# Kernel tuning notes

Hardware: AMD Instinct MI355X
Metric: run time of the kernel (lower is better)

## Reference

```python
import jax, jax.numpy as jnp
import numpy as np

H, D, G, P = 8, 64, 64, 3
ROPE_BASE = 10000.0

def _gelu(x):
    return jax.nn.gelu(x, approximate=False)  # torch nn.GELU default (erf)

def setup_inputs() -> dict:
    key = jax.random.key(0)
    ks = jax.random.split(key, 20)
    B, N, C = 2, 32768, 256
    inner = H * D
    s = 0.02
    inp = {
        'x': jax.random.normal(ks[0], (B, N, C), jnp.float32),
        'pos': jax.random.uniform(ks[1], (B, N, P), jnp.float32),
        'gumbel_u': jax.random.uniform(ks[2], (B, H, N, G), jnp.float32),
        'Wx': jax.random.normal(ks[3], (C, inner), jnp.float32) * s,
        'bx': jnp.zeros((inner,), jnp.float32),
        'W1': jax.random.normal(ks[4], (D, G), jnp.float32) * s,   # proj_temperature[0]
        'b1': jnp.zeros((G,), jnp.float32),
        'W2': jax.random.normal(ks[5], (G, 1), jnp.float32) * s,   # proj_temperature[2]
        'b2': jnp.zeros((1,), jnp.float32),
        'bias': jnp.full((1, H, 1, 1), 0.5, jnp.float32),
        'Wr': jax.random.normal(ks[6], (2 * P, D), jnp.float32) * s,  # rope_projection
        'br': jnp.zeros((D,), jnp.float32),
        'Ws': jax.random.normal(ks[7], (D, G), jnp.float32) * s,   # in_project_slice
        'bs': jnp.zeros((G,), jnp.float32),
        'Wq': jax.random.normal(ks[8], (D, D), jnp.float32) * s,
        'Wk': jax.random.normal(ks[9], (D, D), jnp.float32) * s,
        'Wv': jax.random.normal(ks[10], (D, D), jnp.float32) * s,
        'Wg1': jax.random.normal(ks[11], (2 * D, D), jnp.float32) * s,  # attn_gate[0]
        'bg1': jnp.zeros((D,), jnp.float32),
        'Wg2': jax.random.normal(ks[12], (D, D), jnp.float32) * s,      # attn_gate[2]
        'bg2': jnp.zeros((D,), jnp.float32),
        'Wo': jax.random.normal(ks[13], (inner, C), jnp.float32) * s,   # to_out
        'bo': jnp.zeros((C,), jnp.float32),
    }
    return inp

def reference(x, pos, gumbel_u, Wx, bx, W1, b1, W2, b2, bias, Wr, br, Ws, bs,
              Wq, Wk, Wv, Wg1, bg1, Wg2, bg2, Wo, bo):
    B, N, C = x.shape
    dt = x.dtype
    # project and split heads: [B,H,N,D]
    x_mid = (x @ Wx + bx).reshape(B, N, H, D).transpose(0, 2, 1, 3)
    # RoPE features: sin/cos of pos * inv_freq, projected to dim_head
    inv_freq = jnp.exp(-jnp.arange(P, dtype=dt) * jnp.log(jnp.asarray(ROPE_BASE, dt)) / P)
    ang = pos[..., :P] * inv_freq                                  # [B,N,P]
    rope_feat = jnp.concatenate([jnp.sin(ang), jnp.cos(ang)], -1)  # [B,N,2P]
    x_mid = x_mid + (rope_feat @ Wr + br)[:, None]                 # broadcast over heads
    # per-token temperature, clamped
    temp = _gelu(_gelu(x_mid @ W1 + b1) @ W2 + b2) + bias          # [B,H,N,1]
    temp = jnp.maximum(temp, 0.01)
    # gumbel-softmax slice weights (soft, hard=False)
    logits = x_mid @ Ws + bs                                       # [B,H,N,G]
    gnoise = -jnp.log(-jnp.log(gumbel_u + 1e-8) + 1e-8)
    sw = jax.nn.softmax((logits + gnoise) / temp, axis=-1)
    # pool N tokens into G slice tokens
    snorm = sw.sum(axis=2)                                         # [B,H,G]
    st = jnp.einsum('bhnc,bhng->bhgc', x_mid, sw) / (snorm + 1e-5)[..., None]
    # tiny SDPA over G learned tokens
    q, k, v = st @ Wq, st @ Wk, st @ Wv
    attn = jax.nn.softmax(jnp.einsum('bhgc,bhkc->bhgk', q, k) / jnp.sqrt(jnp.asarray(D, dt)), axis=-1)
    out_st = jnp.einsum('bhgk,bhkc->bhgc', attn, v)
    # sigmoid gate
    gate_in = jnp.concatenate([st, out_st], axis=-1)               # [B,H,G,2D]
    gate = jax.nn.sigmoid(jax.nn.silu(gate_in @ Wg1 + bg1) @ Wg2 + bg2)
    out_st = gate * out_st
    # broadcast slice tokens back to N tokens
    out_x = jnp.einsum('bhgc,bhng->bhnc', out_st, sw)
    out_x = out_x.transpose(0, 2, 1, 3).reshape(B, N, H * D)
    return out_x @ Wo + bo
```

## Files before the change

kernel.cpp:

```cpp
#include <hip/hip_runtime.h>
#include <math.h>

#define NSEQ 32768

using short8v = __attribute__((ext_vector_type(8))) short;
using f32x4   = __attribute__((ext_vector_type(4))) float;
#define MFMA16 __builtin_amdgcn_mfma_f32_16x16x32_bf16

__device__ __forceinline__ unsigned short f2bf(float f){
  union{float f; unsigned u;} v; v.f = f;
  return (unsigned short)((v.u + 0x7FFFu + ((v.u>>16)&1u))>>16);
}
__device__ __forceinline__ float bf2f(unsigned short h){
  union{unsigned u; float f;} v; v.u = ((unsigned)h)<<16; return v.f;
}
__device__ __forceinline__ void split2(float f, unsigned short* h, unsigned short* l){
  unsigned short hh = f2bf(f);
  *h = hh; *l = f2bf(f - bf2f(hh));
}
__device__ __forceinline__ float gelu_f(float x){
  return 0.5f*x*(1.f + erff(x*0.70710678118654752f));
}

__global__ __launch_bounds__(256) void k0_prep(const float* __restrict__ Wx,
    unsigned short* __restrict__ WxTH, unsigned short* __restrict__ WxTL)
{
  const int n = blockIdx.x;
  const int k = threadIdx.x;
  float v = Wx[(size_t)k*512 + n];
  unsigned short hh, ll; split2(v,&hh,&ll);
  WxTH[n*256+k]=hh; WxTL[n*256+k]=ll;
}

__global__ __launch_bounds__(256) void k0b_prep(
  const float* __restrict__ Wq, const float* __restrict__ Wk, const float* __restrict__ Wv,
  const float* __restrict__ Wg1, const float* __restrict__ Wg2, const float* __restrict__ Wo,
  const float* __restrict__ W1, const float* __restrict__ Ws,
  unsigned short* __restrict__ WqTH, unsigned short* __restrict__ WqTL,
  unsigned short* __restrict__ WkTH, unsigned short* __restrict__ WkTL,
  unsigned short* __restrict__ WvTH, unsigned short* __restrict__ WvTL,
  unsigned short* __restrict__ Wg1TH, unsigned short* __restrict__ Wg1TL,
  unsigned short* __restrict__ Wg2TH, unsigned short* __restrict__ Wg2TL,
  unsigned short* __restrict__ WoTH, unsigned short* __restrict__ WoTL,
  unsigned short* __restrict__ W1TH, unsigned short* __restrict__ W1TL,
  unsigned short* __restrict__ WsTH, unsigned short* __restrict__ WsTL)
{
  const int bx = blockIdx.x, t = threadIdx.x;
  unsigned short hh, ll;
  if (bx == 0){
    for (int i=0;i<16;i++){ int idx=i*256+t; int r=idx>>6, c=idx&63;
      split2(Wq[r*64+c],&hh,&ll); WqTH[c*64+r]=hh; WqTL[c*64+r]=ll;
      split2(Wk[r*64+c],&hh,&ll); WkTH[c*64+r]=hh; WkTL[c*64+r]=ll;
      split2(Wv[r*64+c],&hh,&ll); WvTH[c*64+r]=hh; WvTL[c*64+r]=ll;
    }
  } else if (bx == 1){
    for (int i=0;i<32;i++){ int idx=i*256+t; int r=idx>>6, c=idx&63;
      split2(Wg1[r*64+c],&hh,&ll); Wg1TH[c*128+r]=hh; Wg1TL[c*128+r]=ll;
    }
  } else if (bx == 2){
    for (int i=0;i<16;i++){ int idx=i*256+t; int r=idx>>6, c=idx&63;
      split2(Wg2[r*64+c],&hh,&ll); Wg2TH[c*64+r]=hh; Wg2TL[c*64+r]=ll;
      split2(W1[r*64+c],&hh,&ll);  W1TH[c*64+r]=hh;  W1TL[c*64+r]=ll;
      split2(Ws[r*64+c],&hh,&ll);  WsTH[c*64+r]=hh;  WsTL[c*64+r]=ll;
    }
  } else {
    int kb = (bx-3)*64;
    for (int i=0;i<64;i++){ int k = kb+i;
      split2(Wo[(size_t)k*256 + t],&hh,&ll);
      WoTH[(size_t)t*512 + k]=hh; WoTL[(size_t)t*512 + k]=ll;
    }
  }
}

__global__ __launch_bounds__(512,1) void k1_gemm_rope(
    const float* __restrict__ x, const float* __restrict__ pos,
    const unsigned short* __restrict__ WxTH, const unsigned short* __restrict__ WxTL,
    const float* __restrict__ bx,
    const float* __restrict__ Wr, const float* __restrict__ br,
    float* __restrict__ xmid)
{
  __shared__ unsigned short SA[2*128*128];
  __shared__ unsigned short SB[2*64*128];
  __shared__ float trig[128][8];
  const int tid = threadIdx.x;
  const int wave = tid>>6, lane = tid&63, l15 = lane&15, lq = lane>>4;
  const int m0 = blockIdx.x*128;

  if (tid < 128){
    int m = m0 + tid;
    float a0 = pos[m*3+0];
    float a1 = pos[m*3+1] * 0.046415888336127774f;
    float a2 = pos[m*3+2] * 0.002154434690031884f;
    trig[tid][0]=sinf(a0); trig[tid][1]=sinf(a1); trig[tid][2]=sinf(a2);
    trig[tid][3]=cosf(a0); trig[tid][4]=cosf(a1); trig[tid][5]=cosf(a2);
  }

  short8v aHr[8], aLr[8];
  {
    const int lm = tid>>2, lkq = (tid&3)*32;
    #pragma unroll
    for (int kh=0; kh<2; kh++){
      __syncthreads();
      const float* src = x + (size_t)(m0+lm)*256 + kh*128 + lkq;
      #pragma unroll
      for (int i=0;i<8;i++){
        float4 v = *(const float4*)(src + i*4);
        ushort4 hh, ll;
        split2(v.x,&hh.x,&ll.x); split2(v.y,&hh.y,&ll.y);
        split2(v.z,&hh.z,&ll.z); split2(v.w,&hh.w,&ll.w);
        int G = (lkq>>3) + (i>>1);
        int idx = lm*128 + (((G ^ (lm&15)))<<3) + ((i&1)<<2);
        *(ushort4*)&SA[idx] = hh;
        *(ushort4*)&SA[128*128 + idx] = ll;
      }
      __syncthreads();
      const int row = wave*16 + l15;
      #pragma unroll
      for (int ks=0; ks<4; ks++){
        int idx = row*128 + ((((ks<<2)+lq) ^ l15)<<3);
        aHr[kh*4+ks] = *(const short8v*)&SA[idx];
        aLr[kh*4+ks] = *(const short8v*)&SA[128*128 + idx];
      }
    }
  }

  float ropev[4][4];
  #pragma unroll
  for (int r=0;r<4;r++){
    int tk = wave*16 + lq*4 + r;
    float t0=trig[tk][0],t1=trig[tk][1],t2=trig[tk][2];
    float t3=trig[tk][3],t4=trig[tk][4],t5=trig[tk][5];
    #pragma unroll
    for (int j=0;j<4;j++){
      int d = j*16 + l15;
      float v = br[d];
      v = fmaf(t0, Wr[0*64+d], v);
      v = fmaf(t1, Wr[1*64+d], v);
      v = fmaf(t2, Wr[2*64+d], v);
      v = fmaf(t3, Wr[3*64+d], v);
      v = fmaf(t4, Wr[4*64+d], v);
      v = fmaf(t5, Wr[5*64+d], v);
      ropev[r][j] = v;
    }
  }

  const int bidx = m0 >> 15;
  const int nbase = (m0 & 32767) + wave*16 + lq*4;
  const int ln = tid>>3, lnkq = (tid&7)*16;

  for (int h=0; h<8; h++){
    f32x4 acc[4] = {};
    #pragma unroll
    for (int kh=0; kh<2; kh++){
      __syncthreads();
      {
        const unsigned short* sH = WxTH + (size_t)(h*64+ln)*256 + kh*128 + lnkq;
        const unsigned short* sL = WxTL + (size_t)(h*64+ln)*256 + kh*128 + lnkq;
        int g0 = lnkq>>3;
        int i0 = ln*128 + ((g0     ^ (ln&15))<<3);
        int i1 = ln*128 + (((g0+1) ^ (ln&15))<<3);
        *(uint4*)&SB[i0] = *(const uint4*)sH;
        *(uint4*)&SB[i1] = *(const uint4*)(sH+8);
        *(uint4*)&SB[64*128 + i0] = *(const uint4*)sL;
        *(uint4*)&SB[64*128 + i1] = *(const uint4*)(sL+8);
      }
      __syncthreads();
      #pragma unroll
      for (int ks=0; ks<4; ks++){
        short8v a_h = aHr[kh*4+ks], a_l = aLr[kh*4+ks];
        #pragma unroll
        for (int j=0;j<4;j++){
          int idx = (j*16+l15)*128 + ((((ks<<2)+lq) ^ l15)<<3);
          short8v b_h = *(const short8v*)&SB[idx];
          short8v b_l = *(const short8v*)&SB[64*128 + idx];
          acc[j] = MFMA16(a_h,b_h,acc[j],0,0,0);
          acc[j] = MFMA16(a_h,b_l,acc[j],0,0,0);
          acc[j] = MFMA16(a_l,b_h,acc[j],0,0,0);
        }
      }
    }
    #pragma unroll
    for (int j=0;j<4;j++){
      int col = j*16 + l15;
      float bxv = bx[h*64+col];
      #pragma unroll
      for (int r=0;r<4;r++){
        xmid[(((size_t)(bidx*8+h))*NSEQ + nbase + r)*64 + col] =
          acc[j][r] + bxv + ropev[r][j];
      }
    }
  }
}

__global__ __launch_bounds__(512,1) void k2_tile(
  const float* __restrict__ xmid, const float* __restrict__ gum,
  const unsigned short* __restrict__ W1TH, const unsigned short* __restrict__ W1TL,
  const float* __restrict__ b1,
  const float* __restrict__ W2, const float* __restrict__ b2,
  const float* __restrict__ biasp,
  const unsigned short* __restrict__ WsTH, const unsigned short* __restrict__ WsTL,
  const float* __restrict__ bs,
  unsigned* __restrict__ swT, float* __restrict__ part)
{
  __shared__ unsigned short XAh[128*72], XAl[128*72];
  __shared__ unsigned short XBh[64*136], XBl[64*136];
  __shared__ unsigned short swh[64*136], swl[64*136];
  __shared__ float snred[8*64];
  __shared__ float prm[200];

  const int tid = threadIdx.x;
  const int wave = tid>>6, lane = tid&63, l15 = lane&15, lq = lane>>4;
  const int bh = blockIdx.y, chunk = blockIdx.x, h = bh&7;
  const size_t rowbase = (size_t)bh*NSEQ;

  if (tid<64){ prm[tid]=b1[tid]; prm[64+tid]=bs[tid]; prm[128+tid]=W2[tid]; }
  if (tid==64){ prm[192]=b2[0]; prm[193]=biasp[h]; }

  f32x4 acc2[2] = {};
  float snacc[4][4] = {};
  const int gt2 = wave>>1, dbase = (wave&1)*2;

  for (int sub=0; sub<4; ++sub){
    const int n0 = chunk*512 + sub*128;
    __syncthreads();
    {
      const int lm = tid>>2, ldq = (tid&3)*16;
      const float* src = xmid + (rowbase + n0 + lm)*64 + ldq;
      #pragma unroll
      for (int i=0;i<4;i++){
        float4 v = *(const float4*)(src + i*4);
        float vv[4]={v.x,v.y,v.z,v.w};
        ushort4 hh, ll;
        unsigned short* hp=(unsigned short*)&hh; unsigned short* lp=(unsigned short*)&ll;
        #pragma unroll
        for (int j=0;j<4;j++) split2(vv[j], &hp[j], &lp[j]);
        *(ushort4*)&XAh[lm*72 + ldq + i*4] = hh;
        *(ushort4*)&XAl[lm*72 + ldq + i*4] = ll;
        #pragma unroll
        for (int j=0;j<4;j++){
          XBh[(ldq+i*4+j)*136 + lm] = hp[j];
          XBl[(ldq+i*4+j)*136 + lm] = lp[j];
        }
      }
    }
    __syncthreads();

    const int mloc = wave*16 + l15;
    const float* grow = gum + (rowbase + n0 + mloc)*64;
    float4 gu[4];
    #pragma unroll
    for (int gt=0; gt<4; gt++) gu[gt] = *(const float4*)(grow + gt*16 + lq*4);

    f32x4 t1a[4] = {}, lga[4] = {};
    #pragma unroll
    for (int ks=0; ks<2; ks++){
      const int koff = ks*32 + lq*8;
      short8v xH = *(const short8v*)&XAh[(wave*16+l15)*72 + koff];
      short8v xL = *(const short8v*)&XAl[(wave*16+l15)*72 + koff];
      #pragma unroll
      for (int gt=0; gt<4; gt++){
        const int woff = (gt*16+l15)*64 + koff;
        short8v wH = *(const short8v*)(W1TH + woff);
        short8v wL = *(const short8v*)(W1TL + woff);
        t1a[gt] = MFMA16(wH,xH,t1a[gt],0,0,0);
        t1a[gt] = MFMA16(wH,xL,t1a[gt],0,0,0);
        t1a[gt] = MFMA16(wL,xH,t1a[gt],0,0,0);
        short8v sH = *(const short8v*)(WsTH + woff);
        short8v sL = *(const short8v*)(WsTL + woff);
        lga[gt] = MFMA16(sH,xH,lga[gt],0,0,0);
        lga[gt] = MFMA16(sH,xL,lga[gt],0,0,0);
        lga[gt] = MFMA16(sL,xH,lga[gt],0,0,0);
      }
    }

    float p = 0.f;
    #pragma unroll
    for (int gt=0; gt<4; gt++)
      #pragma unroll
      for (int r=0;r<4;r++){
        int g = gt*16 + lq*4 + r;
        p += gelu_f(t1a[gt][r] + prm[g]) * prm[128+g];
      }
    p += __shfl_xor(p,16); p += __shfl_xor(p,32);
    float t2 = gelu_f(p + prm[192]);
    float rtemp = 1.f / fmaxf(t2 + prm[193], 0.01f);

    float z[4][4]; float mx = -1e30f;
    #pragma unroll
    for (int gt=0; gt<4; gt++){
      float guv[4] = {gu[gt].x, gu[gt].y, gu[gt].z, gu[gt].w};
      #pragma unroll
      for (int r=0;r<4;r++){
        int g = gt*16 + lq*4 + r;
        float gn = -__logf(-__logf(guv[r]+1e-8f)+1e-8f);
        float zz = (lga[gt][r] + prm[64+g] + gn)*rtemp;
        z[gt][r]=zz; mx = fmaxf(mx, zz);
      }
    }
    mx = fmaxf(mx, __shfl_xor(mx,16)); mx = fmaxf(mx, __shfl_xor(mx,32));
    float se = 0.f;
    #pragma unroll
    for (int gt=0; gt<4; gt++)
      #pragma unroll
      for (int r=0;r<4;r++){ float e = __expf(z[gt][r]-mx); z[gt][r]=e; se += e; }
    se += __shfl_xor(se,16); se += __shfl_xor(se,32);
    float inv = 1.f/se;
    #pragma unroll
    for (int gt=0; gt<4; gt++)
      #pragma unroll
      for (int r=0;r<4;r++){
        float swv = z[gt][r]*inv;
        snacc[gt][r] += swv;
        int g = gt*16 + lq*4 + r;
        unsigned short hh,ll; split2(swv,&hh,&ll);
        swh[g*136 + mloc] = hh; swl[g*136 + mloc] = ll;
      }
    __syncthreads();

    {
      const int g = tid>>3, mq = (tid&7)*16;
      #pragma unroll
      for (int i=0;i<4;i++){
        ushort4 hh = *(const ushort4*)&swh[g*136 + mq + i*4];
        ushort4 ll = *(const ushort4*)&swl[g*136 + mq + i*4];
        uint4 pk;
        pk.x = (unsigned)hh.x | ((unsigned)ll.x<<16);
        pk.y = (unsigned)hh.y | ((unsigned)ll.y<<16);
        pk.z = (unsigned)hh.z | ((unsigned)ll.z<<16);
        pk.w = (unsigned)hh.w | ((unsigned)ll.w<<16);
        *(uint4*)(swT + ((size_t)bh*64 + g)*NSEQ + n0 + mq + i*4) = pk;
      }
    }

    #pragma unroll
    for (int ks=0; ks<4; ks++){
      const int koff = ks*32 + lq*8;
      short8v aH = *(const short8v*)&swh[(gt2*16+l15)*136 + koff];
      short8v aL = *(const short8v*)&swl[(gt2*16+l15)*136 + koff];
      #pragma unroll
      for (int dt=0; dt<2; dt++){
        const int boff = ((dbase+dt)*16+l15)*136 + koff;
        short8v bH = *(const short8v*)&XBh[boff];
        short8v bL = *(const short8v*)&XBl[boff];
        acc2[dt] = MFMA16(aH,bH,acc2[dt],0,0,0);
        acc2[dt] = MFMA16(aH,bL,acc2[dt],0,0,0);
        acc2[dt] = MFMA16(aL,bH,acc2[dt],0,0,0);
      }
    }
  }

  float* pb = part + ((size_t)bh*64 + chunk)*4160;
  #pragma unroll
  for (int dt=0; dt<2; dt++)
    #pragma unroll
    for (int r=0;r<4;r++){
      int g = gt2*16 + lq*4 + r;
      int d = (dbase+dt)*16 + l15;
      pb[g*64 + d] = acc2[dt][r];
    }
  #pragma unroll
  for (int gt=0; gt<4; gt++)
    #pragma unroll
    for (int r=0;r<4;r++){
      float v = snacc[gt][r];
      v += __shfl_xor(v,1); v += __shfl_xor(v,2);
      v += __shfl_xor(v,4); v += __shfl_xor(v,8);
      if (l15==0) snred[wave*64 + gt*16 + lq*4 + r] = v;
    }
  __syncthreads();
  if (tid < 64){
    float s = 0.f;
    #pragma unroll
    for (int w=0; w<8; w++) s += snred[w*64 + tid];
    pb[4096 + tid] = s;
  }
}

__global__ __launch_bounds__(256) void k3a_reduce(
    const float* __restrict__ part, float* __restrict__ stred)
{
  const int bh = blockIdx.x;
  const int i = blockIdx.y*256 + threadIdx.x;
  if (i >= 4160) return;
  const float* pb = part + (size_t)bh*64*4160 + i;
  float s[8] = {};
  #pragma unroll 2
  for (int c=0; c<64; c+=8)
    #pragma unroll
    for (int j=0;j<8;j++) s[j] += pb[(size_t)(c+j)*4160];
  stred[bh*4160 + i] = ((s[0]+s[1])+(s[2]+s[3])) + ((s[4]+s[5])+(s[6]+s[7]));
}

__global__ __launch_bounds__(256) void k3b_slice(
    const float* __restrict__ stred,
    const unsigned short* __restrict__ WqTH, const unsigned short* __restrict__ WqTL,
    const unsigned short* __restrict__ WkTH, const unsigned short* __restrict__ WkTL,
    const unsigned short* __restrict__ WvTH, const unsigned short* __restrict__ WvTL,
    const unsigned short* __restrict__ Wg1TH, const unsigned short* __restrict__ Wg1TL,
    const unsigned short* __restrict__ Wg2TH, const unsigned short* __restrict__ Wg2TL,
    const unsigned short* __restrict__ WoTH, const unsigned short* __restrict__ WoTL,
    const float* __restrict__ bg1, const float* __restrict__ bg2,
    float* __restrict__ Mt)
{
  __shared__ unsigned short stH[64*72], stL[64*72];
  __shared__ unsigned short qH[64*72],  qL[64*72];
  __shared__ unsigned short kH[64*72],  kL[64*72];
  __shared__ unsigned short vTH[64*72], vTL[64*72];
  __shared__ unsigned short pH[64*72],  pL[64*72];
  __shared__ unsigned short oH[64*72],  oL[64*72];
  __shared__ unsigned short h1H[64*72], h1L[64*72];
  __shared__ unsigned short gH[64*72],  gL[64*72];
  __shared__ float snl[64];

  const int tid = threadIdx.x;
  const int wave = tid>>6, lane = tid&63, l15 = lane&15, lq = lane>>4;
  const int bh = blockIdx.x, h = bh&7;
  const int grow = wave*16 + lq*4;

  if (tid < 64) snl[tid] = stred[bh*4160 + 4096 + tid] + 1e-5f;
  __syncthreads();
  {
    const int g = tid>>2, doff = (tid&3)*16;
    const float sn = snl[g];
    #pragma unroll
    for (int i=0;i<4;i++){
      float4 v = *(const float4*)(stred + bh*4160 + g*64 + doff + i*4);
      ushort4 hh, ll;
      split2(v.x/sn,&hh.x,&ll.x); split2(v.y/sn,&hh.y,&ll.y);
      split2(v.z/sn,&hh.z,&ll.z); split2(v.w/sn,&hh.w,&ll.w);
      *(ushort4*)&stH[g*72 + doff + i*4] = hh;
      *(ushort4*)&stL[g*72 + doff + i*4] = ll;
    }
  }
  __syncthreads();

  {
    f32x4 aq[4]={}, ak[4]={}, av[4]={};
    #pragma unroll
    for (int ks=0; ks<2; ks++){
      const int koff = ks*32 + lq*8;
      short8v sH = *(const short8v*)&stH[(wave*16+l15)*72 + koff];
      short8v sL = *(const short8v*)&stL[(wave*16+l15)*72 + koff];
      #pragma unroll
      for (int j=0;j<4;j++){
        const int boff = (j*16+l15)*64 + koff;
        short8v bH, bL;
        bH = *(const short8v*)(WqTH+boff); bL = *(const short8v*)(WqTL+boff);
        aq[j]=MFMA16(sH,bH,aq[j],0,0,0); aq[j]=MFMA16(sH,bL,aq[j],0,0,0); aq[j]=MFMA16(sL,bH,aq[j],0,0,0);
        bH = *(const short8v*)(WkTH+boff); bL = *(const short8v*)(WkTL+boff);
        ak[j]=MFMA16(sH,bH,ak[j],0,0,0); ak[j]=MFMA16(sH,bL,ak[j],0,0,0); ak[j]=MFMA16(sL,bH,ak[j],0,0,0);
        bH = *(const short8v*)(WvTH+boff); bL = *(const short8v*)(WvTL+boff);
        av[j]=MFMA16(sH,bH,av[j],0,0,0); av[j]=MFMA16(sH,bL,av[j],0,0,0); av[j]=MFMA16(sL,bH,av[j],0,0,0);
      }
    }
    #pragma unroll
    for (int j=0;j<4;j++){
      #pragma unroll
      for (int r=0;r<4;r++){
        unsigned short hh,ll;
        split2(aq[j][r],&hh,&ll); qH[(grow+r)*72 + j*16+l15]=hh; qL[(grow+r)*72 + j*16+l15]=ll;
        split2(ak[j][r],&hh,&ll); kH[(grow+r)*72 + j*16+l15]=hh; kL[(grow+r)*72 + j*16+l15]=ll;
        split2(av[j][r],&hh,&ll); vTH[(j*16+l15)*72 + grow+r]=hh; vTL[(j*16+l15)*72 + grow+r]=ll;
      }
    }
  }
  __syncthreads();

  {
    f32x4 sc[4]={};
    #pragma unroll
    for (int ks=0; ks<2; ks++){
      const int koff = ks*32 + lq*8;
      short8v aHf = *(const short8v*)&qH[(wave*16+l15)*72 + koff];
      short8v aLf = *(const short8v*)&qL[(wave*16+l15)*72 + koff];
      #pragma unroll
      for (int jt=0; jt<4; jt++){
        const int boff = (jt*16+l15)*72 + koff;
        short8v bH = *(const short8v*)&kH[boff];
        short8v bL = *(const short8v*)&kL[boff];
        sc[jt]=MFMA16(aHf,bH,sc[jt],0,0,0); sc[jt]=MFMA16(aHf,bL,sc[jt],0,0,0); sc[jt]=MFMA16(aLf,bH,sc[jt],0,0,0);
      }
    }
    #pragma unroll
    for (int r=0;r<4;r++){
      float s0=sc[0][r]*0.125f, s1=sc[1][r]*0.125f, s2=sc[2][r]*0.125f, s3=sc[3][r]*0.125f;
      float mx = fmaxf(fmaxf(s0,s1),fmaxf(s2,s3));
      mx=fmaxf(mx,__shfl_xor(mx,1)); mx=fmaxf(mx,__shfl_xor(mx,2));
      mx=fmaxf(mx,__shfl_xor(mx,4)); mx=fmaxf(mx,__shfl_xor(mx,8));
      float e0=__expf(s0-mx), e1=__expf(s1-mx), e2=__expf(s2-mx), e3=__expf(s3-mx);
      float se = e0+e1+e2+e3;
      se+=__shfl_xor(se,1); se+=__shfl_xor(se,2); se+=__shfl_xor(se,4); se+=__shfl_xor(se,8);
      float inv = 1.f/se;
      sc[0][r]=e0*inv; sc[1][r]=e1*inv; sc[2][r]=e2*inv; sc[3][r]=e3*inv;
    }
    #pragma unroll
    for (int jt=0; jt<4; jt++)
      #pragma unroll
      for (int r=0;r<4;r++){
        unsigned short hh,ll; split2(sc[jt][r],&hh,&ll);
        pH[(grow+r)*72 + jt*16+l15]=hh; pL[(grow+r)*72 + jt*16+l15]=ll;
      }
  }
  __syncthreads();

  f32x4 os[4] = {};
  {
    #pragma unroll
    for (int ks=0; ks<2; ks++){
      const int koff = ks*32 + lq*8;
      short8v aHf = *(const short8v*)&pH[(wave*16+l15)*72 + koff];
      short8v aLf = *(const short8v*)&pL[(wave*16+l15)*72 + koff];
      #pragma unroll
      for (int dt=0; dt<4; dt++){
        const int boff = (dt*16+l15)*72 + koff;
        short8v bH = *(const short8v*)&vTH[boff];
        short8v bL = *(const short8v*)&vTL[boff];
        os[dt]=MFMA16(aHf,bH,os[dt],0,0,0); os[dt]=MFMA16(aHf,bL,os[dt],0,0,0); os[dt]=MFMA16(aLf,bH,os[dt],0,0,0);
      }
    }
    #pragma unroll
    for (int dt=0; dt<4; dt++)
      #pragma unroll
      for (int r=0;r<4;r++){
        unsigned short hh,ll; split2(os[dt][r],&hh,&ll);
        oH[(grow+r)*72 + dt*16+l15]=hh; oL[(grow+r)*72 + dt*16+l15]=ll;
      }
  }
  __syncthreads();

  {
    f32x4 ha[4] = {};
    #pragma unroll
    for (int ks=0; ks<4; ks++){
      const int koff2 = (ks&1)*32 + lq*8;
      short8v aHf, aLf;
      if (ks<2){ aHf = *(const short8v*)&stH[(wave*16+l15)*72 + koff2];
                 aLf = *(const short8v*)&stL[(wave*16+l15)*72 + koff2]; }
      else     { aHf = *(const short8v*)&oH[(wave*16+l15)*72 + koff2];
                 aLf = *(const short8v*)&oL[(wave*16+l15)*72 + koff2]; }
      #pragma unroll
      for (int dt=0; dt<4; dt++){
        const int boff = (dt*16+l15)*128 + ks*32 + lq*8;
        short8v bH = *(const short8v*)(Wg1TH+boff);
        short8v bL = *(const short8v*)(Wg1TL+boff);
        ha[dt]=MFMA16(aHf,bH,ha[dt],0,0,0); ha[dt]=MFMA16(aHf,bL,ha[dt],0,0,0); ha[dt]=MFMA16(aLf,bH,ha[dt],0,0,0);
      }
    }
    #pragma unroll
    for (int dt=0; dt<4; dt++){
      float bg = bg1[dt*16+l15];
      #pragma unroll
      for (int r=0;r<4;r++){
        float s = ha[dt][r] + bg;
        float sv = s/(1.f+__expf(-s));
        unsigned short hh,ll; split2(sv,&hh,&ll);
        h1H[(grow+r)*72 + dt*16+l15]=hh; h1L[(grow+r)*72 + dt*16+l15]=ll;
      }
    }
  }
  __syncthreads();

  {
    f32x4 ga[4] = {};
    #pragma unroll
    for (int ks=0; ks<2; ks++){
      const int koff = ks*32 + lq*8;
      short8v aHf = *(const short8v*)&h1H[(wave*16+l15)*72 + koff];
      short8v aLf = *(const short8v*)&h1L[(wave*16+l15)*72 + koff];
      #pragma unroll
      for (int dt=0; dt<4; dt++){
        const int boff = (dt*16+l15)*64 + koff;
        short8v bH = *(const short8v*)(Wg2TH+boff);
        short8v bL = *(const short8v*)(Wg2TL+boff);
        ga[dt]=MFMA16(aHf,bH,ga[dt],0,0,0); ga[dt]=MFMA16(aHf,bL,ga[dt],0,0,0); ga[dt]=MFMA16(aLf,bH,ga[dt],0,0,0);
      }
    }
    #pragma unroll
    for (int dt=0; dt<4; dt++){
      float bg = bg2[dt*16+l15];
      #pragma unroll
      for (int r=0;r<4;r++){
        float gate = 1.f/(1.f+__expf(-(ga[dt][r]+bg)));
        float gv = gate * os[dt][r];
        unsigned short hh,ll; split2(gv,&hh,&ll);
        gH[(grow+r)*72 + dt*16+l15]=hh; gL[(grow+r)*72 + dt*16+l15]=ll;
      }
    }
  }
  __syncthreads();

  {
    f32x4 mac[16] = {};
    #pragma unroll
    for (int ks=0; ks<2; ks++){
      const int koff = ks*32 + lq*8;
      short8v aHf = *(const short8v*)&gH[(wave*16+l15)*72 + koff];
      short8v aLf = *(const short8v*)&gL[(wave*16+l15)*72 + koff];
      #pragma unroll
      for (int ct=0; ct<16; ct++){
        const size_t boff = (size_t)(ct*16+l15)*512 + h*64 + koff;
        short8v bH = *(const short8v*)(WoTH+boff);
        short8v bL = *(const short8v*)(WoTL+boff);
        mac[ct]=MFMA16(aHf,bH,mac[ct],0,0,0); mac[ct]=MFMA16(aHf,bL,mac[ct],0,0,0); mac[ct]=MFMA16(aLf,bH,mac[ct],0,0,0);
      }
    }
    #pragma unroll
    for (int ct=0; ct<16; ct++)
      #pragma unroll
      for (int r=0;r<4;r++)
        Mt[(size_t)bh*16384 + (size_t)(ct*16+l15)*64 + grow + r] = mac[ct][r];
  }
}

__global__ __launch_bounds__(256,2) void k4_out(
  const unsigned* __restrict__ swT, const float* __restrict__ Mt,
  const float* __restrict__ bo, float* __restrict__ out)
{
  __shared__ unsigned short AH[64*72], AL[64*72];
  __shared__ unsigned short BH[128*72], BL[128*72];
  const int tid = threadIdx.x;
  const int wave = tid>>6, lane = tid&63, l15 = lane&15, lq = lane>>4;
  const int m0 = blockIdx.x*64, c0 = blockIdx.y*128;
  const int b = m0>>15, nn = m0 & 32767;
  f32x4 acc[8] = {};

  for (int hh=0; hh<8; hh++){
    const int bhh = b*8 + hh;
    __syncthreads();
    {
      const int g = tid>>2, mq = (tid&3)*16;
      const unsigned* src = swT + ((size_t)bhh*64 + g)*NSEQ + nn + mq;
      #pragma unroll
      for (int i=0;i<4;i++){
        uint4 pv = *(const uint4*)(src + i*4);
        unsigned u[4]={pv.x,pv.y,pv.z,pv.w};
        #pragma unroll
        for (int j=0;j<4;j++){
          int m = mq + i*4 + j;
          AH[m*72+g] = (unsigned short)(u[j] & 0xFFFFu);
          AL[m*72+g] = (unsigned short)(u[j] >> 16);
        }
      }
      const int c = tid>>1, gq = (tid&1)*32;
      const float* bsrc = Mt + (size_t)bhh*16384 + (size_t)(c0+c)*64 + gq;
      #pragma unroll
      for (int i=0;i<8;i++){
        float4 v = *(const float4*)(bsrc + i*4);
        float vv[4]={v.x,v.y,v.z,v.w};
        ushort4 hh4, ll4;
        unsigned short* hp=(unsigned short*)&hh4; unsigned short* lp=(unsigned short*)&ll4;
        #pragma unroll
        for (int j=0;j<4;j++) split2(vv[j], &hp[j], &lp[j]);
        *(ushort4*)&BH[c*72 + gq + i*4] = hh4;
        *(ushort4*)&BL[c*72 + gq + i*4] = ll4;
      }
    }
    __syncthreads();
    #pragma unroll
    for (int ks=0; ks<2; ks++){
      const int koff = ks*32 + lq*8;
      short8v aH = *(const short8v*)&AH[(wave*16+l15)*72 + koff];
      short8v aL = *(const short8v*)&AL[(wave*16+l15)*72 + koff];
      #pragma unroll
      for (int ct=0; ct<8; ct++){
        short8v bH = *(const short8v*)&BH[(ct*16+l15)*72 + koff];
        short8v bL = *(const short8v*)&BL[(ct*16+l15)*72 + koff];
        acc[ct] = MFMA16(aH,bH,acc[ct],0,0,0);
        acc[ct] = MFMA16(aH,bL,acc[ct],0,0,0);
        acc[ct] = MFMA16(aL,bH,acc[ct],0,0,0);
      }
    }
  }
  #pragma unroll
  for (int ct=0; ct<8; ct++)
    #pragma unroll
    for (int r=0;r<4;r++){
      int c = c0 + ct*16 + l15;
      out[(size_t)(m0 + wave*16 + lq*4 + r)*256 + c] = acc[ct][r] + bo[c];
    }
}

extern "C" void kernel_launch(void* const* d_in, const int* in_sizes, int n_in,
                              void* d_out, int out_size, void* d_ws, size_t ws_size,
                              hipStream_t stream) {
  (void)in_sizes; (void)n_in; (void)out_size;
  const float* x    = (const float*)d_in[0];
  const float* pos  = (const float*)d_in[1];
  const float* gum  = (const float*)d_in[2];
  const float* Wx   = (const float*)d_in[3];
  const float* bx   = (const float*)d_in[4];
  const float* W1   = (const float*)d_in[5];
  const float* b1   = (const float*)d_in[6];
  const float* W2   = (const float*)d_in[7];
  const float* b2   = (const float*)d_in[8];
  const float* bias = (const float*)d_in[9];
  const float* Wr   = (const float*)d_in[10];
  const float* br   = (const float*)d_in[11];
  const float* Ws   = (const float*)d_in[12];
  const float* bs   = (const float*)d_in[13];
  const float* Wq   = (const float*)d_in[14];
  const float* Wk   = (const float*)d_in[15];
  const float* Wv   = (const float*)d_in[16];
  const float* Wg1  = (const float*)d_in[17];
  const float* bg1  = (const float*)d_in[18];
  const float* Wg2  = (const float*)d_in[19];
  const float* bg2  = (const float*)d_in[20];
  const float* Wo   = (const float*)d_in[21];
  const float* bo   = (const float*)d_in[22];
  float* out = (float*)d_out;

  float*    xmid  = (float*)d_ws;
  unsigned* swT   = (unsigned*)(xmid + (size_t)33554432);
  float*    partp = (float*)(swT + (size_t)33554432);
  float*    stred = partp + (size_t)4259840;
  unsigned short* WxTH = (unsigned short*)(stred + (size_t)66560);
  unsigned short* WxTL  = WxTH + (size_t)131072;
  unsigned short* WqTH  = WxTL + (size_t)131072;
  unsigned short* WqTL  = WqTH + 4096;
  unsigned short* WkTH  = WqTL + 4096;
  unsigned short* WkTL  = WkTH + 4096;
  unsigned short* WvTH  = WkTL + 4096;
  unsigned short* WvTL  = WvTH + 4096;
  unsigned short* Wg1TH = WvTL + 4096;
  unsigned short* Wg1TL = Wg1TH + 8192;
  unsigned short* Wg2TH = Wg1TL + 8192;
  unsigned short* Wg2TL = Wg2TH + 4096;
  unsigned short* WoTH  = Wg2TL + 4096;
  unsigned short* WoTL  = WoTH + (size_t)131072;
  unsigned short* W1TH  = WoTL + (size_t)131072;
  unsigned short* W1TL  = W1TH + 4096;
  unsigned short* WsTH  = W1TL + 4096;
  unsigned short* WsTL  = WsTH + 4096;
  float*    Mt    = partp;
  const size_t need = ((size_t)33554432*2 + 4259840 + 66560)*4 + (size_t)589824*2;
  if (ws_size < need) return;

  k0_prep<<<512, 256, 0, stream>>>(Wx, WxTH, WxTL);
  k0b_prep<<<11, 256, 0, stream>>>(Wq, Wk, Wv, Wg1, Wg2, Wo, W1, Ws,
      WqTH,WqTL,WkTH,WkTL,WvTH,WvTL,Wg1TH,Wg1TL,Wg2TH,Wg2TL,WoTH,WoTL,W1TH,W1TL,WsTH,WsTL);
  k1_gemm_rope<<<512, 512, 0, stream>>>(x, pos, WxTH, WxTL, bx, Wr, br, xmid);
  k2_tile<<<dim3(64,16), 512, 0, stream>>>(xmid, gum, W1TH, W1TL, b1, W2, b2, bias, WsTH, WsTL, bs, swT, partp);
  k3a_reduce<<<dim3(16,17), 256, 0, stream>>>(partp, stred);
  k3b_slice<<<16, 256, 0, stream>>>(stred, WqTH,WqTL,WkTH,WkTL,WvTH,WvTL,
      Wg1TH,Wg1TL,Wg2TH,Wg2TL,WoTH,WoTL, bg1, bg2, Mt);
  k4_out<<<dim3(1024,2), 256, 0, stream>>>(swT, Mt, bo, out);
}
```

Baseline: 479.6 us.

## Stage W1/Ws in LDS, swizzle transposed X tile, pre-split Mt to bf16 pairs

In k2_tile, the W1 and Ws hi/lo weights are now loaded once per block into shared memory instead of being re-read from global memory on every MFMA operand fetch. The transposed X tile (XB) moves to an XOR-swizzled 128-wide layout written with vector stores, which is meant to cut LDS bank conflicts and scalar stores. k3b now writes Mt already split into packed bf16 hi/lo pairs, so k4_out skips the per-element split in its inner loop. The cost is extra LDS in k2, which could lower occupancy, plus a more complex indexing scheme.

```diff
diff --git a/kernel.cpp b/kernel.cpp
--- a/kernel.cpp
+++ b/kernel.cpp
@@ -203,7 +203,9 @@
   unsigned* __restrict__ swT, float* __restrict__ part)
 {
   __shared__ unsigned short XAh[128*72], XAl[128*72];
-  __shared__ unsigned short XBh[64*136], XBl[64*136];
+  __shared__ unsigned short XBh[64*128], XBl[64*128];
+  __shared__ unsigned short W1h[64*72], W1l[64*72];
+  __shared__ unsigned short Wsh[64*72], Wsl[64*72];
   __shared__ unsigned short swh[64*136], swl[64*136];
   __shared__ float snred[8*64];
   __shared__ float prm[200];
@@ -213,6 +215,13 @@
   const int bh = blockIdx.y, chunk = blockIdx.x, h = bh&7;
   const size_t rowbase = (size_t)bh*NSEQ;
 
+  {
+    const int g = tid>>3, c8 = (tid&7)*8;
+    *(uint4*)&W1h[g*72+c8] = *(const uint4*)(W1TH + g*64 + c8);
+    *(uint4*)&W1l[g*72+c8] = *(const uint4*)(W1TL + g*64 + c8);
+    *(uint4*)&Wsh[g*72+c8] = *(const uint4*)(WsTH + g*64 + c8);
+    *(uint4*)&Wsl[g*72+c8] = *(const uint4*)(WsTL + g*64 + c8);
+  }
   if (tid<64){ prm[tid]=b1[tid]; prm[64+tid]=bs[tid]; prm[128+tid]=W2[tid]; }
   if (tid==64){ prm[192]=b2[0]; prm[193]=biasp[h]; }
 
@@ -224,23 +233,28 @@
     const int n0 = chunk*512 + sub*128;
     __syncthreads();
     {
-      const int lm = tid>>2, ldq = (tid&3)*16;
-      const float* src = xmid + (rowbase + n0 + lm)*64 + ldq;
+      const int mq = (tid>>4)*4, dq = (tid&15)*4;
+      const float* src = xmid + (rowbase + n0 + mq)*64 + dq;
+      unsigned short hh[4][4], ll[4][4];
       #pragma unroll
       for (int i=0;i<4;i++){
-        float4 v = *(const float4*)(src + i*4);
-        float vv[4]={v.x,v.y,v.z,v.w};
-        ushort4 hh, ll;
-        unsigned short* hp=(unsigned short*)&hh; unsigned short* lp=(unsigned short*)&ll;
-        #pragma unroll
-        for (int j=0;j<4;j++) split2(vv[j], &hp[j], &lp[j]);
-        *(ushort4*)&XAh[lm*72 + ldq + i*4] = hh;
-        *(ushort4*)&XAl[lm*72 + ldq + i*4] = ll;
-        #pragma unroll
-        for (int j=0;j<4;j++){
-          XBh[(ldq+i*4+j)*136 + lm] = hp[j];
-          XBl[(ldq+i*4+j)*136 + lm] = lp[j];
-        }
+        float4 v = *(const float4*)(src + i*64);
+        split2(v.x,&hh[i][0],&ll[i][0]); split2(v.y,&hh[i][1],&ll[i][1]);
+        split2(v.z,&hh[i][2],&ll[i][2]); split2(v.w,&hh[i][3],&ll[i][3]);
+        ushort4 th; th.x=hh[i][0]; th.y=hh[i][1]; th.z=hh[i][2]; th.w=hh[i][3];
+        ushort4 tl; tl.x=ll[i][0]; tl.y=ll[i][1]; tl.z=ll[i][2]; tl.w=ll[i][3];
+        *(ushort4*)&XAh[(mq+i)*72 + dq] = th;
+        *(ushort4*)&XAl[(mq+i)*72 + dq] = tl;
+      }
+      const int gm = mq>>3, mh = mq&7;
+      #pragma unroll
+      for (int j=0;j<4;j++){
+        int d = dq+j;
+        int base = d*128 + ((gm ^ (d&15))<<3) + mh;
+        ushort4 th; th.x=hh[0][j]; th.y=hh[1][j]; th.z=hh[2][j]; th.w=hh[3][j];
+        ushort4 tl; tl.x=ll[0][j]; tl.y=ll[1][j]; tl.z=ll[2][j]; tl.w=ll[3][j];
+        *(ushort4*)&XBh[base] = th;
+        *(ushort4*)&XBl[base] = tl;
       }
     }
     __syncthreads();
@@ -259,14 +273,14 @@
       short8v xL = *(const short8v*)&XAl[(wave*16+l15)*72 + koff];
       #pragma unroll
       for (int gt=0; gt<4; gt++){
-        const int woff = (gt*16+l15)*64 + koff;
-        short8v wH = *(const short8v*)(W1TH + woff);
-        short8v wL = *(const short8v*)(W1TL + woff);
+        const int aoff = (gt*16+l15)*72 + koff;
+        short8v wH = *(const short8v*)&W1h[aoff];
+        short8v wL = *(const short8v*)&W1l[aoff];
         t1a[gt] = MFMA16(wH,xH,t1a[gt],0,0,0);
         t1a[gt] = MFMA16(wH,xL,t1a[gt],0,0,0);
         t1a[gt] = MFMA16(wL,xH,t1a[gt],0,0,0);
-        short8v sH = *(const short8v*)(WsTH + woff);
-        short8v sL = *(const short8v*)(WsTL + woff);
+        short8v sH = *(const short8v*)&Wsh[aoff];
+        short8v sL = *(const short8v*)&Wsl[aoff];
         lga[gt] = MFMA16(sH,xH,lga[gt],0,0,0);
         lga[gt] = MFMA16(sH,xL,lga[gt],0,0,0);
         lga[gt] = MFMA16(sL,xH,lga[gt],0,0,0);
@@ -337,9 +351,11 @@
       const int koff = ks*32 + lq*8;
       short8v aH = *(const short8v*)&swh[(gt2*16+l15)*136 + koff];
       short8v aL = *(const short8v*)&swl[(gt2*16+l15)*136 + koff];
+      const int gran = ks*4 + lq;
       #pragma unroll
       for (int dt=0; dt<2; dt++){
-        const int boff = ((dbase+dt)*16+l15)*136 + koff;
+        const int d = (dbase+dt)*16 + l15;
+        const int boff = d*128 + ((gran ^ (d&15))<<3);
         short8v bH = *(const short8v*)&XBh[boff];
         short8v bL = *(const short8v*)&XBl[boff];
         acc2[dt] = MFMA16(aH,bH,acc2[dt],0,0,0);
@@ -400,7 +416,7 @@
     const unsigned short* __restrict__ Wg2TH, const unsigned short* __restrict__ Wg2TL,
     const unsigned short* __restrict__ WoTH, const unsigned short* __restrict__ WoTL,
     const float* __restrict__ bg1, const float* __restrict__ bg2,
-    float* __restrict__ Mt)
+    unsigned* __restrict__ MtP)
 {
   __shared__ unsigned short stH[64*72], stL[64*72];
   __shared__ unsigned short qH[64*72],  qL[64*72];
@@ -607,13 +623,16 @@
     #pragma unroll
     for (int ct=0; ct<16; ct++)
       #pragma unroll
-      for (int r=0;r<4;r++)
-        Mt[(size_t)bh*16384 + (size_t)(ct*16+l15)*64 + grow + r] = mac[ct][r];
+      for (int r=0;r<4;r++){
+        unsigned short hh,ll; split2(mac[ct][r],&hh,&ll);
+        MtP[(size_t)bh*16384 + (size_t)(ct*16+l15)*64 + grow + r] =
+          (unsigned)hh | ((unsigned)ll<<16);
+      }
   }
 }
 
 __global__ __launch_bounds__(256,2) void k4_out(
-  const unsigned* __restrict__ swT, const float* __restrict__ Mt,
+  const unsigned* __restrict__ swT, const unsigned* __restrict__ MtP,
   const float* __restrict__ bo, float* __restrict__ out)
 {
   __shared__ unsigned short AH[64*72], AL[64*72];
@@ -642,15 +661,15 @@
         }
       }
       const int c = tid>>1, gq = (tid&1)*32;
-      const float* bsrc = Mt + (size_t)bhh*16384 + (size_t)(c0+c)*64 + gq;
+      const unsigned* bsrc = MtP + (size_t)bhh*16384 + (size_t)(c0+c)*64 + gq;
       #pragma unroll
       for (int i=0;i<8;i++){
-        float4 v = *(const float4*)(bsrc + i*4);
-        float vv[4]={v.x,v.y,v.z,v.w};
+        uint4 pv = *(const uint4*)(bsrc + i*4);
         ushort4 hh4, ll4;
-        unsigned short* hp=(unsigned short*)&hh4; unsigned short* lp=(unsigned short*)&ll4;
-        #pragma unroll
-        for (int j=0;j<4;j++) split2(vv[j], &hp[j], &lp[j]);
+        hh4.x=(unsigned short)(pv.x&0xFFFFu); ll4.x=(unsigned short)(pv.x>>16);
+        hh4.y=(unsigned short)(pv.y&0xFFFFu); ll4.y=(unsigned short)(pv.y>>16);
+        hh4.z=(unsigned short)(pv.z&0xFFFFu); ll4.z=(unsigned short)(pv.z>>16);
+        hh4.w=(unsigned short)(pv.w&0xFFFFu); ll4.w=(unsigned short)(pv.w>>16);
         *(ushort4*)&BH[c*72 + gq + i*4] = hh4;
         *(ushort4*)&BL[c*72 + gq + i*4] = ll4;
       }
@@ -731,7 +750,7 @@
   unsigned short* W1TL  = W1TH + 4096;
   unsigned short* WsTH  = W1TL + 4096;
   unsigned short* WsTL  = WsTH + 4096;
-  float*    Mt    = partp;
+  unsigned* MtP = (unsigned*)partp;
   const size_t need = ((size_t)33554432*2 + 4259840 + 66560)*4 + (size_t)589824*2;
   if (ws_size < need) return;
 
@@ -742,6 +761,6 @@
   k2_tile<<<dim3(64,16), 512, 0, stream>>>(xmid, gum, W1TH, W1TL, b1, W2, b2, bias, WsTH, WsTL, bs, swT, partp);
   k3a_reduce<<<dim3(16,17), 256, 0, stream>>>(partp, stred);
   k3b_slice<<<16, 256, 0, stream>>>(stred, WqTH,WqTL,WkTH,WkTL,WvTH,WvTL,
-      Wg1TH,Wg1TL,Wg2TH,Wg2TL,WoTH,WoTL, bg1, bg2, Mt);
-  k4_out<<<dim3(1024,2), 256, 0, stream>>>(swT, Mt, bo, out);
-}
+      Wg1TH,Wg1TL,Wg2TH,Wg2TL,WoTH,WoTL, bg1, bg2, MtP);
+  k4_out<<<dim3(1024,2), 256, 0, stream>>>(swT, MtP, bo, out);
+}
```

Result: faster. 418.0 us (-12.8%).
